# Performance work log

Hardware: AMD Instinct MI355X
Metric: run time of the kernel (lower is better)

The kernel has to match this reference:

```python
import jax, jax.numpy as jnp
import numpy as np

R, H, K, C = 8, 8, 4096, 128  # residual stages, subvectors, codebook size, subvector dim
B, S = 2, 2048


def setup_inputs() -> dict:
    key = jax.random.key(0)
    k1, k2 = jax.random.split(key)
    x = jax.random.normal(k1, (B, S, H * C), dtype=jnp.float32)
    codebook = jax.random.normal(k2, (R, H, K, C), dtype=jnp.float32) * 0.1
    return {"x": x, "codebook": codebook}


def _encode(x, codebook):
    b, s, f = x.shape
    # x.view(b,s,8,2,64).transpose(3,4).flatten(2)  -> interleave the two 64-dim halves per head
    xp = x.reshape(b, s, 8, 2, 64).transpose(0, 1, 2, 4, 3).reshape(b, s, f)
    prescale = jnp.linalg.norm(xp, axis=-1, keepdims=True)  # (b,s,1)
    xn = xp / prescale
    # (b s) h c  -> permute to (h, N, c)
    t0 = xn.reshape(b * s, H, C).transpose(1, 0, 2)  # (H, N, C)

    def step(t, cb_r):
        # cb_r: (H, K, C). Squared-euclidean argmin == torch.cdist argmin (sqrt is monotone,
        # and the ||t||^2 term is constant over k so it is dropped).
        d = jnp.sum(cb_r * cb_r, axis=-1)[:, None, :] - 2.0 * jnp.einsum('hnc,hkc->hnk', t, cb_r)
        idx = jnp.argmin(d, axis=-1)  # (H, N)
        q = jnp.take_along_axis(cb_r, idx[..., None], axis=1)  # (H, N, C)
        return t - q, idx.astype(jnp.int32)

    _, codes = jax.lax.scan(step, t0, codebook)  # codes: (R, H, N)
    return codes, prescale


def _decode(codes, prescale, codebook):
    # gather codebook entries: (R, H, N, C)
    g = jnp.take_along_axis(codebook, codes[..., None], axis=2)
    n = codes.shape[2]
    # permute(0,2,1,3).flatten(-2).sum(0): (R,N,H*C) summed over residual stages
    rec = g.transpose(0, 2, 1, 3).reshape(R, n, H * C).sum(0)  # (N, H*C)
    b = prescale.shape[0]
    return rec.reshape(b, -1, H * C) * prescale


def reference(x, codebook):
    codes, prescale = _encode(x, codebook)
    return _decode(codes, prescale, codebook)
```

## Files before the change

### kernel.cpp

```cpp
#include <hip/hip_runtime.h>

#define R_STAGES 8
#define H_HEADS  8
#define K_CODES  4096
#define C_DIM    128
#define N_TOK    4096
#define FEAT     1024
#define HKC      (H_HEADS * K_CODES * C_DIM)

#define MARGIN   1e-2f
#define PCAP     16

typedef _Float16 half8  __attribute__((ext_vector_type(8)));
typedef _Float16 half4v __attribute__((ext_vector_type(4)));
typedef float    f32x4  __attribute__((ext_vector_type(4)));

#define MFMA16(A, B, C) __builtin_amdgcn_mfma_f32_16x16x32_f16((A), (B), (C), 0, 0, 0)


__global__ void kc_prep(const float* __restrict__ x, float* __restrict__ t,
                        float* __restrict__ ps) {
    int n = blockIdx.x;
    const float* xr = x + (size_t)n * FEAT;

    double ss = 0.0;
    for (int i = threadIdx.x; i < FEAT; i += 256) {
        float v = xr[i];
        ss += (double)v * (double)v;
    }
    for (int off = 32; off > 0; off >>= 1) ss += __shfl_down(ss, off);

    __shared__ double sred[4];
    __shared__ float s_p;
    int wid = threadIdx.x >> 6, lane = threadIdx.x & 63;
    if (lane == 0) sred[wid] = ss;
    __syncthreads();
    if (threadIdx.x == 0) {
        double tot = sred[0] + sred[1] + sred[2] + sred[3];
        float p = (float)sqrt(tot);
        ps[n] = p;
        s_p = p;
    }
    __syncthreads();
    float p = s_p;

    for (int i = threadIdx.x; i < FEAT; i += 256) {
        int c = i & 127;
        float v = xr[(i & ~127) + ((c & 1) << 6) + (c >> 1)];
        size_t o = ((size_t)(i >> 7) * N_TOK + n) * C_DIM + c;
        t[o] = v / p;
    }
}

__global__ void kc_cbn(const float* __restrict__ cb, float* __restrict__ cn) {
    int w = (blockIdx.x << 2) + (threadIdx.x >> 6);
    int lane = threadIdx.x & 63;
    const float* row = cb + (size_t)w * C_DIM;
    float a = row[lane], b = row[lane + 64];
    double s = (double)a * a + (double)b * b;
    for (int off = 32; off > 0; off >>= 1) s += __shfl_down(s, off);
    if (lane == 0) cn[w] = (float)s;
}

__global__ void kc_cvt(const float* __restrict__ s, _Float16* __restrict__ d, int n4) {
    int i = blockIdx.x * 256 + threadIdx.x;
    if (i < n4) {
        f32x4 v = ((const f32x4*)s)[i];
        half4v o;
        o[0] = (_Float16)v[0]; o[1] = (_Float16)v[1];
        o[2] = (_Float16)v[2]; o[3] = (_Float16)v[3];
        ((half4v*)d)[i] = o;
    }
}

__global__ __launch_bounds__(256, 2)
void kc_stage(const float* __restrict__ cb32, const _Float16* __restrict__ cb16,
              const float* __restrict__ cn, float* __restrict__ t) {
    __shared__ float  rbs[256][4];
    __shared__ float  mtok[64];
    __shared__ int    pcnt[64];
    __shared__ int    plist[64][PCAP];
    __shared__ int    winner[64];
    __shared__ double redD[256];
    __shared__ int    redI[256];

    const int tid  = threadIdx.x;
    const int w    = tid >> 6;
    const int lane = tid & 63;
    const int col  = lane & 15;
    const int rblk = lane >> 4;
    const int h    = blockIdx.x & 7;
    const int n0   = (blockIdx.x >> 3) << 6;

    const _Float16* cbh16 = cb16 + (size_t)h * K_CODES * C_DIM;
    const float*    cbh32 = cb32 + (size_t)h * K_CODES * C_DIM;
    const float*    cnh   = cn   + (size_t)h * K_CODES;
    float* th = t + ((size_t)h * N_TOK + n0) * C_DIM;

    if (tid < 64) pcnt[tid] = 0;

    half8 tf[4][4];
#pragma unroll
    for (int g = 0; g < 4; ++g) {
        const float* trow = th + (size_t)(g * 16 + col) * C_DIM;
#pragma unroll
        for (int j = 0; j < 4; ++j) {
            const float* p = trow + j * 32 + rblk * 8;
            f32x4 lo = *(const f32x4*)p;
            f32x4 hi = *(const f32x4*)(p + 4);
            half8 v;
            v[0] = (_Float16)lo[0]; v[1] = (_Float16)lo[1];
            v[2] = (_Float16)lo[2]; v[3] = (_Float16)lo[3];
            v[4] = (_Float16)hi[0]; v[5] = (_Float16)hi[1];
            v[6] = (_Float16)hi[2]; v[7] = (_Float16)hi[3];
            tf[g][j] = v;
        }
    }

    const int kbase = w << 10;
    const _Float16* cbA = cbh16 + (size_t)(kbase + col) * C_DIM + rblk * 8;
    const float*    cnA = cnh + kbase + (rblk << 2);

    auto loadA = [&](int it, half8* A, f32x4& cv) {
        const _Float16* p = cbA + (size_t)it * (16 * C_DIM);
#pragma unroll
        for (int j = 0; j < 4; ++j) A[j] = *(const half8*)(p + j * 32);
        cv = *(const f32x4*)(cnA + it * 16);
    };

    float rb0 = 3.4e38f, rb1 = 3.4e38f, rb2 = 3.4e38f, rb3 = 3.4e38f;

    auto screen = [&](const half8* A, const f32x4& cv) {
        f32x4 a0 = {0.f,0.f,0.f,0.f}, a1 = {0.f,0.f,0.f,0.f};
        f32x4 a2 = {0.f,0.f,0.f,0.f}, a3 = {0.f,0.f,0.f,0.f};
#pragma unroll
        for (int j = 0; j < 4; ++j) {
            a0 = MFMA16(A[j], tf[0][j], a0);
            a1 = MFMA16(A[j], tf[1][j], a1);
            a2 = MFMA16(A[j], tf[2][j], a2);
            a3 = MFMA16(A[j], tf[3][j], a3);
        }
        {
            float d0 = cv[0] - 2.f*a0[0], d1 = cv[1] - 2.f*a0[1];
            float d2 = cv[2] - 2.f*a0[2], d3 = cv[3] - 2.f*a0[3];
            rb0 = fminf(rb0, fminf(fminf(d0, d1), fminf(d2, d3)));
        }
        {
            float d0 = cv[0] - 2.f*a1[0], d1 = cv[1] - 2.f*a1[1];
            float d2 = cv[2] - 2.f*a1[2], d3 = cv[3] - 2.f*a1[3];
            rb1 = fminf(rb1, fminf(fminf(d0, d1), fminf(d2, d3)));
        }
        {
            float d0 = cv[0] - 2.f*a2[0], d1 = cv[1] - 2.f*a2[1];
            float d2 = cv[2] - 2.f*a2[2], d3 = cv[3] - 2.f*a2[3];
            rb2 = fminf(rb2, fminf(fminf(d0, d1), fminf(d2, d3)));
        }
        {
            float d0 = cv[0] - 2.f*a3[0], d1 = cv[1] - 2.f*a3[1];
            float d2 = cv[2] - 2.f*a3[2], d3 = cv[3] - 2.f*a3[3];
            rb3 = fminf(rb3, fminf(fminf(d0, d1), fminf(d2, d3)));
        }
    };

    {
        half8 X[4], Y[4]; f32x4 cx, cy;
        loadA(0, X, cx);
#pragma unroll 1
        for (int it = 0; it < 64; it += 2) {
            loadA(it + 1, Y, cy);
            screen(X, cx);
            if (it + 2 < 64) loadA(it + 2, X, cx);
            screen(Y, cy);
        }
    }

    rbs[tid][0] = rb0; rbs[tid][1] = rb1; rbs[tid][2] = rb2; rbs[tid][3] = rb3;
    __syncthreads();
    if (tid < 64) {
        int g = tid >> 4, c2 = tid & 15;
        float m = 3.4e38f;
#pragma unroll
        for (int ww = 0; ww < 4; ++ww)
#pragma unroll
            for (int rr = 0; rr < 4; ++rr)
                m = fminf(m, rbs[ww * 64 + rr * 16 + c2][g]);
        mtok[tid] = m;
    }
    __syncthreads();

    const float thr0 = mtok[col]      + MARGIN;
    const float thr1 = mtok[16 + col] + MARGIN;
    const float thr2 = mtok[32 + col] + MARGIN;
    const float thr3 = mtok[48 + col] + MARGIN;

    auto collect = [&](const half8* A, const f32x4& cv, int it) {
        f32x4 a0 = {0.f,0.f,0.f,0.f}, a1 = {0.f,0.f,0.f,0.f};
        f32x4 a2 = {0.f,0.f,0.f,0.f}, a3 = {0.f,0.f,0.f,0.f};
#pragma unroll
        for (int j = 0; j < 4; ++j) {
            a0 = MFMA16(A[j], tf[0][j], a0);
            a1 = MFMA16(A[j], tf[1][j], a1);
            a2 = MFMA16(A[j], tf[2][j], a2);
            a3 = MFMA16(A[j], tf[3][j], a3);
        }
        const int kb2 = kbase + it * 16 + (rblk << 2);
#pragma unroll
        for (int rr = 0; rr < 4; ++rr) {
            float d0 = cv[rr] - 2.f * a0[rr];
            float d1 = cv[rr] - 2.f * a1[rr];
            float d2 = cv[rr] - 2.f * a2[rr];
            float d3 = cv[rr] - 2.f * a3[rr];
            if (d0 < thr0) { int idx = atomicAdd(&pcnt[col],      1); if (idx < PCAP) plist[col][idx]      = kb2 + rr; }
            if (d1 < thr1) { int idx = atomicAdd(&pcnt[16 + col], 1); if (idx < PCAP) plist[16 + col][idx] = kb2 + rr; }
            if (d2 < thr2) { int idx = atomicAdd(&pcnt[32 + col], 1); if (idx < PCAP) plist[32 + col][idx] = kb2 + rr; }
            if (d3 < thr3) { int idx = atomicAdd(&pcnt[48 + col], 1); if (idx < PCAP) plist[48 + col][idx] = kb2 + rr; }
        }
    };

    {
        half8 X[4], Y[4]; f32x4 cx, cy;
        loadA(0, X, cx);
#pragma unroll 1
        for (int it = 0; it < 64; it += 2) {
            loadA(it + 1, Y, cy);
            collect(X, cx, it);
            if (it + 2 < 64) loadA(it + 2, X, cx);
            collect(Y, cy, it + 1);
        }
    }
    __syncthreads();

    {
        const int tok = tid >> 2, q = tid & 3;
        int m = pcnt[tok]; if (m > PCAP) m = PCAP;
        const float* trw = th + (size_t)tok * C_DIM;
        double bd = 1e300; int bi = 0x7fffffff;
        for (int e = q; e < m; e += 4) {
            const int k = plist[tok][e];
            const float* crow = cbh32 + (size_t)k * C_DIM;
            double dot = 0.0, cx2 = 0.0;
            for (int c = 0; c < C_DIM; ++c) {
                double cvv = (double)crow[c];
                double tvv = (double)trw[c];
                cx2 = fma(cvv, cvv, cx2);
                dot = fma(tvv, cvv, dot);
            }
            double d = cx2 - 2.0 * dot;
            if (d < bd || (d == bd && k < bi)) { bd = d; bi = k; }
        }
        redD[tid] = bd; redI[tid] = bi;
    }
    __syncthreads();
    if ((tid & 3) == 0) {
        const int tok = tid >> 2;
        double bd = redD[tid]; int bi = redI[tid];
#pragma unroll
        for (int q = 1; q < 4; ++q) {
            double d = redD[tid + q]; int i2 = redI[tid + q];
            if (d < bd || (d == bd && i2 < bi)) { bd = d; bi = i2; }
        }
        winner[tok] = bi;
    }
    __syncthreads();

    for (int ot = 0; ot < 64; ++ot) {
        if (pcnt[ot] <= PCAP) continue;
        const float* trw = th + (size_t)ot * C_DIM;
        double bd = 1e300; int bi = 0x7fffffff;
        for (int k = tid; k < K_CODES; k += 256) {
            const float* crow = cbh32 + (size_t)k * C_DIM;
            double dot = 0.0, cx2 = 0.0;
            for (int c = 0; c < C_DIM; ++c) {
                double cvv = (double)crow[c];
                double tvv = (double)trw[c];
                cx2 = fma(cvv, cvv, cx2);
                dot = fma(tvv, cvv, dot);
            }
            double d = cx2 - 2.0 * dot;
            if (d < bd || (d == bd && k < bi)) { bd = d; bi = k; }
        }
        for (int off = 32; off > 0; off >>= 1) {
            double od = __shfl_down(bd, off);
            int    oi = __shfl_down(bi, off);
            if (od < bd || (od == bd && oi < bi)) { bd = od; bi = oi; }
        }
        if (lane == 0) { redD[w] = bd; redI[w] = bi; }
        __syncthreads();
        if (tid == 0) {
            double b2 = redD[0]; int i2 = redI[0];
            for (int q = 1; q < 4; ++q) {
                if (redD[q] < b2 || (redD[q] == b2 && redI[q] < i2)) {
                    b2 = redD[q]; i2 = redI[q];
                }
            }
            winner[ot] = i2;
        }
        __syncthreads();
    }

    for (int i = tid; i < 64 * C_DIM; i += 256) {
        const int tok = i >> 7, c = i & 127;
        const float qv = cbh32[(size_t)winner[tok] * C_DIM + c];
        th[(size_t)tok * C_DIM + c] -= qv;
    }
}

__global__ void kc_out(const float* __restrict__ x, const float* __restrict__ t,
                       const float* __restrict__ ps, float* __restrict__ out) {
    int n = blockIdx.x;
    float p = ps[n];
    const float* xr = x + (size_t)n * FEAT;
    for (int i = threadIdx.x; i < FEAT; i += 256) {
        int c = i & 127;
        float v = xr[(i & ~127) + ((c & 1) << 6) + (c >> 1)];
        float t0 = v / p;
        float tf = t[((size_t)(i >> 7) * N_TOK + n) * C_DIM + c];
        out[(size_t)n * FEAT + i] = (t0 - tf) * p;
    }
}

extern "C" void kernel_launch(void* const* d_in, const int* in_sizes, int n_in,
                              void* d_out, int out_size, void* d_ws, size_t ws_size,
                              hipStream_t stream) {
    const float* x  = (const float*)d_in[0];
    const float* cb = (const float*)d_in[1];
    float* out = (float*)d_out;

    float*    t    = (float*)d_ws;
    float*    ps   = (float*)((char*)d_ws + 16777216);
    float*    cn   = (float*)((char*)d_ws + 16793600);
    _Float16* cb16 = (_Float16*)((char*)d_ws + 17842176);

    const bool full = (ws_size >= 51500000ull);

    kc_prep<<<N_TOK, 256, 0, stream>>>(x, t, ps);
    kc_cbn<<<(R_STAGES * H_HEADS * K_CODES) / 4, 256, 0, stream>>>(cb, cn);
    if (full) {
        const int n4 = R_STAGES * HKC / 4;
        kc_cvt<<<(n4 + 255) / 256, 256, 0, stream>>>(cb, cb16, n4);
    }

    for (int r = 0; r < R_STAGES; ++r) {
        const _Float16* cb16s;
        if (full) {
            cb16s = cb16 + (size_t)r * HKC;
        } else {
            const int n4 = HKC / 4;
            kc_cvt<<<(n4 + 255) / 256, 256, 0, stream>>>(cb + (size_t)r * HKC, cb16, n4);
            cb16s = cb16;
        }
        kc_stage<<<H_HEADS * (N_TOK / 64), 256, 0, stream>>>(
            cb + (size_t)r * HKC, cb16s,
            cn + (size_t)r * H_HEADS * K_CODES, t);
    }
    kc_out<<<N_TOK, 256, 0, stream>>>(x, t, ps, out);
}
```

Baseline: 1.223 ms.

## Replace second MFMA pass with per-tile min cache and fuse all stages into one kernel

The screening pass now stores a per-16-code-tile minimum distance for each token in shared memory. Candidate tiles are then picked from that cache instead of recomputing all distances in a second MFMA collect pass, and only those tiles are rescored in double precision. All residual stages run inside one persistent kernel per token-block, removing per-stage launches, and codebook fp16 conversion is fused with norm computation. This adds a large shared-memory buffer, which may reduce occupancy. It also falls back to full brute-force rescoring whenever the candidate list overflows.

```diff
diff --git a/kernel.cpp b/kernel.cpp
--- a/kernel.cpp
+++ b/kernel.cpp
@@ -8,8 +8,9 @@
 #define FEAT     1024
 #define HKC      (H_HEADS * K_CODES * C_DIM)
 
-#define MARGIN   1e-2f
-#define PCAP     16
+#define MARGIN   1.2e-2f
+#define WCAP     512
+#define TMS      260
 
 typedef _Float16 half8  __attribute__((ext_vector_type(8)));
 typedef _Float16 half4v __attribute__((ext_vector_type(4)));
@@ -52,52 +53,40 @@
     }
 }
 
-__global__ void kc_cbn(const float* __restrict__ cb, float* __restrict__ cn) {
+__global__ void kc_cvtn(const float* __restrict__ cb, _Float16* __restrict__ cb16,
+                        float* __restrict__ cn) {
     int w = (blockIdx.x << 2) + (threadIdx.x >> 6);
     int lane = threadIdx.x & 63;
     const float* row = cb + (size_t)w * C_DIM;
     float a = row[lane], b = row[lane + 64];
+    _Float16* dr = cb16 + (size_t)w * C_DIM;
+    dr[lane]      = (_Float16)a;
+    dr[lane + 64] = (_Float16)b;
     double s = (double)a * a + (double)b * b;
     for (int off = 32; off > 0; off >>= 1) s += __shfl_down(s, off);
     if (lane == 0) cn[w] = (float)s;
 }
 
-__global__ void kc_cvt(const float* __restrict__ s, _Float16* __restrict__ d, int n4) {
-    int i = blockIdx.x * 256 + threadIdx.x;
-    if (i < n4) {
-        f32x4 v = ((const f32x4*)s)[i];
-        half4v o;
-        o[0] = (_Float16)v[0]; o[1] = (_Float16)v[1];
-        o[2] = (_Float16)v[2]; o[3] = (_Float16)v[3];
-        ((half4v*)d)[i] = o;
-    }
-}
-
-__global__ __launch_bounds__(256, 2)
-void kc_stage(const float* __restrict__ cb32, const _Float16* __restrict__ cb16,
-              const float* __restrict__ cn, float* __restrict__ t) {
-    __shared__ float  rbs[256][4];
-    __shared__ float  mtok[64];
-    __shared__ int    pcnt[64];
-    __shared__ int    plist[64][PCAP];
-    __shared__ int    winner[64];
-    __shared__ double redD[256];
-    __shared__ int    redI[256];
+__device__ __forceinline__ void stage_body(
+    const float* __restrict__ cbh32, const _Float16* __restrict__ cbh16,
+    const float* __restrict__ cnh, float* __restrict__ th) {
+
+    __shared__ _Float16 tmin[64 * TMS];
+    __shared__ float    rbs[256][4];
+    __shared__ float    mtok[64];
+    __shared__ int      wl[WCAP];
+    __shared__ double   eD[WCAP];
+    __shared__ int      eI[WCAP];
+    __shared__ int      winner[64];
+    __shared__ int      wlCnt;
 
     const int tid  = threadIdx.x;
     const int w    = tid >> 6;
     const int lane = tid & 63;
     const int col  = lane & 15;
     const int rblk = lane >> 4;
-    const int h    = blockIdx.x & 7;
-    const int n0   = (blockIdx.x >> 3) << 6;
-
-    const _Float16* cbh16 = cb16 + (size_t)h * K_CODES * C_DIM;
-    const float*    cbh32 = cb32 + (size_t)h * K_CODES * C_DIM;
-    const float*    cnh   = cn   + (size_t)h * K_CODES;
-    float* th = t + ((size_t)h * N_TOK + n0) * C_DIM;
-
-    if (tid < 64) pcnt[tid] = 0;
+
+    if (tid == 0) wlCnt = 0;
 
     half8 tf[4][4];
 #pragma unroll
@@ -128,9 +117,9 @@
         cv = *(const f32x4*)(cnA + it * 16);
     };
 
-    float rb0 = 3.4e38f, rb1 = 3.4e38f, rb2 = 3.4e38f, rb3 = 3.4e38f;
-
-    auto screen = [&](const half8* A, const f32x4& cv) {
+    float rbg0 = 3.4e38f, rbg1 = 3.4e38f, rbg2 = 3.4e38f, rbg3 = 3.4e38f;
+
+    auto screen = [&](const half8* A, const f32x4& cv, int wtile) {
         f32x4 a0 = {0.f,0.f,0.f,0.f}, a1 = {0.f,0.f,0.f,0.f};
         f32x4 a2 = {0.f,0.f,0.f,0.f}, a3 = {0.f,0.f,0.f,0.f};
 #pragma unroll
@@ -140,169 +129,188 @@
             a2 = MFMA16(A[j], tf[2][j], a2);
             a3 = MFMA16(A[j], tf[3][j], a3);
         }
-        {
-            float d0 = cv[0] - 2.f*a0[0], d1 = cv[1] - 2.f*a0[1];
-            float d2 = cv[2] - 2.f*a0[2], d3 = cv[3] - 2.f*a0[3];
-            rb0 = fminf(rb0, fminf(fminf(d0, d1), fminf(d2, d3)));
-        }
-        {
-            float d0 = cv[0] - 2.f*a1[0], d1 = cv[1] - 2.f*a1[1];
-            float d2 = cv[2] - 2.f*a1[2], d3 = cv[3] - 2.f*a1[3];
-            rb1 = fminf(rb1, fminf(fminf(d0, d1), fminf(d2, d3)));
-        }
-        {
-            float d0 = cv[0] - 2.f*a2[0], d1 = cv[1] - 2.f*a2[1];
-            float d2 = cv[2] - 2.f*a2[2], d3 = cv[3] - 2.f*a2[3];
-            rb2 = fminf(rb2, fminf(fminf(d0, d1), fminf(d2, d3)));
-        }
-        {
-            float d0 = cv[0] - 2.f*a3[0], d1 = cv[1] - 2.f*a3[1];
-            float d2 = cv[2] - 2.f*a3[2], d3 = cv[3] - 2.f*a3[3];
-            rb3 = fminf(rb3, fminf(fminf(d0, d1), fminf(d2, d3)));
+        float m0 = fminf(fminf(cv[0] - 2.f*a0[0], cv[1] - 2.f*a0[1]),
+                         fminf(cv[2] - 2.f*a0[2], cv[3] - 2.f*a0[3]));
+        float m1 = fminf(fminf(cv[0] - 2.f*a1[0], cv[1] - 2.f*a1[1]),
+                         fminf(cv[2] - 2.f*a1[2], cv[3] - 2.f*a1[3]));
+        float m2 = fminf(fminf(cv[0] - 2.f*a2[0], cv[1] - 2.f*a2[1]),
+                         fminf(cv[2] - 2.f*a2[2], cv[3] - 2.f*a2[3]));
+        float m3 = fminf(fminf(cv[0] - 2.f*a3[0], cv[1] - 2.f*a3[1]),
+                         fminf(cv[2] - 2.f*a3[2], cv[3] - 2.f*a3[3]));
+        m0 = fminf(m0, __shfl_xor(m0, 16)); m0 = fminf(m0, __shfl_xor(m0, 32));
+        m1 = fminf(m1, __shfl_xor(m1, 16)); m1 = fminf(m1, __shfl_xor(m1, 32));
+        m2 = fminf(m2, __shfl_xor(m2, 16)); m2 = fminf(m2, __shfl_xor(m2, 32));
+        m3 = fminf(m3, __shfl_xor(m3, 16)); m3 = fminf(m3, __shfl_xor(m3, 32));
+        rbg0 = fminf(rbg0, m0); rbg1 = fminf(rbg1, m1);
+        rbg2 = fminf(rbg2, m2); rbg3 = fminf(rbg3, m3);
+        if (rblk == 0) {
+            tmin[(col)      * TMS + wtile] = (_Float16)m0;
+            tmin[(16 + col) * TMS + wtile] = (_Float16)m1;
+            tmin[(32 + col) * TMS + wtile] = (_Float16)m2;
+            tmin[(48 + col) * TMS + wtile] = (_Float16)m3;
         }
     };
 
     {
-        half8 X[4], Y[4]; f32x4 cx, cy;
-        loadA(0, X, cx);
+        half8 A0[4], A1[4], A2[4], A3[4];
+        f32x4 v0, v1, v2, v3;
+        loadA(0, A0, v0); loadA(1, A1, v1); loadA(2, A2, v2); loadA(3, A3, v3);
+        const int wbase = w << 6;
 #pragma unroll 1
-        for (int it = 0; it < 64; it += 2) {
-            loadA(it + 1, Y, cy);
-            screen(X, cx);
-            if (it + 2 < 64) loadA(it + 2, X, cx);
-            screen(Y, cy);
-        }
-    }
-
-    rbs[tid][0] = rb0; rbs[tid][1] = rb1; rbs[tid][2] = rb2; rbs[tid][3] = rb3;
-    __syncthreads();
+        for (int j = 0; j < 16; ++j) {
+            const int b4 = j << 2;
+            screen(A0, v0, wbase + b4);
+            if (j < 15) loadA(b4 + 4, A0, v0);
+            screen(A1, v1, wbase + b4 + 1);
+            if (j < 15) loadA(b4 + 5, A1, v1);
+            screen(A2, v2, wbase + b4 + 2);
+            if (j < 15) loadA(b4 + 6, A2, v2);
+            screen(A3, v3, wbase + b4 + 3);
+            if (j < 15) loadA(b4 + 7, A3, v3);
+        }
+    }
+    rbs[tid][0] = rbg0; rbs[tid][1] = rbg1; rbs[tid][2] = rbg2; rbs[tid][3] = rbg3;
+    __syncthreads();
+
     if (tid < 64) {
-        int g = tid >> 4, c2 = tid & 15;
+        const int g = tid >> 4, c2 = tid & 15;
         float m = 3.4e38f;
 #pragma unroll
-        for (int ww = 0; ww < 4; ++ww)
-#pragma unroll
-            for (int rr = 0; rr < 4; ++rr)
-                m = fminf(m, rbs[ww * 64 + rr * 16 + c2][g]);
+        for (int ww = 0; ww < 4; ++ww) m = fminf(m, rbs[ww * 64 + c2][g]);
         mtok[tid] = m;
-    }
-    __syncthreads();
-
-    const float thr0 = mtok[col]      + MARGIN;
-    const float thr1 = mtok[16 + col] + MARGIN;
-    const float thr2 = mtok[32 + col] + MARGIN;
-    const float thr3 = mtok[48 + col] + MARGIN;
-
-    auto collect = [&](const half8* A, const f32x4& cv, int it) {
-        f32x4 a0 = {0.f,0.f,0.f,0.f}, a1 = {0.f,0.f,0.f,0.f};
-        f32x4 a2 = {0.f,0.f,0.f,0.f}, a3 = {0.f,0.f,0.f,0.f};
-#pragma unroll
-        for (int j = 0; j < 4; ++j) {
-            a0 = MFMA16(A[j], tf[0][j], a0);
-            a1 = MFMA16(A[j], tf[1][j], a1);
-            a2 = MFMA16(A[j], tf[2][j], a2);
-            a3 = MFMA16(A[j], tf[3][j], a3);
-        }
-        const int kb2 = kbase + it * 16 + (rblk << 2);
-#pragma unroll
-        for (int rr = 0; rr < 4; ++rr) {
-            float d0 = cv[rr] - 2.f * a0[rr];
-            float d1 = cv[rr] - 2.f * a1[rr];
-            float d2 = cv[rr] - 2.f * a2[rr];
-            float d3 = cv[rr] - 2.f * a3[rr];
-            if (d0 < thr0) { int idx = atomicAdd(&pcnt[col],      1); if (idx < PCAP) plist[col][idx]      = kb2 + rr; }
-            if (d1 < thr1) { int idx = atomicAdd(&pcnt[16 + col], 1); if (idx < PCAP) plist[16 + col][idx] = kb2 + rr; }
-            if (d2 < thr2) { int idx = atomicAdd(&pcnt[32 + col], 1); if (idx < PCAP) plist[32 + col][idx] = kb2 + rr; }
-            if (d3 < thr3) { int idx = atomicAdd(&pcnt[48 + col], 1); if (idx < PCAP) plist[48 + col][idx] = kb2 + rr; }
-        }
-    };
-
-    {
-        half8 X[4], Y[4]; f32x4 cx, cy;
-        loadA(0, X, cx);
-#pragma unroll 1
-        for (int it = 0; it < 64; it += 2) {
-            loadA(it + 1, Y, cy);
-            collect(X, cx, it);
-            if (it + 2 < 64) loadA(it + 2, X, cx);
-            collect(Y, cy, it + 1);
-        }
     }
     __syncthreads();
 
     {
         const int tok = tid >> 2, q = tid & 3;
-        int m = pcnt[tok]; if (m > PCAP) m = PCAP;
-        const float* trw = th + (size_t)tok * C_DIM;
-        double bd = 1e300; int bi = 0x7fffffff;
-        for (int e = q; e < m; e += 4) {
-            const int k = plist[tok][e];
-            const float* crow = cbh32 + (size_t)k * C_DIM;
-            double dot = 0.0, cx2 = 0.0;
-            for (int c = 0; c < C_DIM; ++c) {
-                double cvv = (double)crow[c];
-                double tvv = (double)trw[c];
-                cx2 = fma(cvv, cvv, cx2);
-                dot = fma(tvv, cvv, dot);
-            }
-            double d = cx2 - 2.0 * dot;
-            if (d < bd || (d == bd && k < bi)) { bd = d; bi = k; }
-        }
-        redD[tid] = bd; redI[tid] = bi;
-    }
-    __syncthreads();
-    if ((tid & 3) == 0) {
-        const int tok = tid >> 2;
-        double bd = redD[tid]; int bi = redI[tid];
-#pragma unroll
-        for (int q = 1; q < 4; ++q) {
-            double d = redD[tid + q]; int i2 = redI[tid + q];
-            if (d < bd || (d == bd && i2 < bi)) { bd = d; bi = i2; }
-        }
-        winner[tok] = bi;
-    }
-    __syncthreads();
-
-    for (int ot = 0; ot < 64; ++ot) {
-        if (pcnt[ot] <= PCAP) continue;
-        const float* trw = th + (size_t)ot * C_DIM;
-        double bd = 1e300; int bi = 0x7fffffff;
-        for (int k = tid; k < K_CODES; k += 256) {
-            const float* crow = cbh32 + (size_t)k * C_DIM;
-            double dot = 0.0, cx2 = 0.0;
-            for (int c = 0; c < C_DIM; ++c) {
-                double cvv = (double)crow[c];
-                double tvv = (double)trw[c];
-                cx2 = fma(cvv, cvv, cx2);
-                dot = fma(tvv, cvv, dot);
-            }
-            double d = cx2 - 2.0 * dot;
-            if (d < bd || (d == bd && k < bi)) { bd = d; bi = k; }
-        }
-        for (int off = 32; off > 0; off >>= 1) {
-            double od = __shfl_down(bd, off);
-            int    oi = __shfl_down(bi, off);
-            if (od < bd || (od == bd && oi < bi)) { bd = od; bi = oi; }
-        }
-        if (lane == 0) { redD[w] = bd; redI[w] = bi; }
+        const float thr = mtok[tok] + MARGIN;
+        const half4v* rowp = (const half4v*)(tmin + tok * TMS + (q << 6));
+#pragma unroll 4
+        for (int j4 = 0; j4 < 16; ++j4) {
+            half4v v = rowp[j4];
+#pragma unroll
+            for (int e = 0; e < 4; ++e) {
+                if ((float)v[e] < thr) {
+                    int idx = atomicAdd(&wlCnt, 1);
+                    if (idx < WCAP) wl[idx] = (tok << 8) | ((q << 6) + (j4 << 2) + e);
+                }
+            }
+        }
+    }
+    __syncthreads();
+
+    int E = wlCnt;
+    if (E <= WCAP) {
+        for (int e0 = 0; e0 < E; e0 += 16) {
+            const int e = e0 + (tid >> 4);
+            double bd = 1e300; int bi = 0x7fffffff;
+            if (e < E) {
+                const int meta = wl[e];
+                const int tok = meta >> 8;
+                const int k = ((meta & 255) << 4) + (tid & 15);
+                const float* crow = cbh32 + (size_t)k * C_DIM;
+                const float* trw  = th + (size_t)tok * C_DIM;
+                double cx0=0,cx1=0,cx2=0,cx3=0,d0=0,d1=0,d2=0,d3=0;
+#pragma unroll 4
+                for (int c = 0; c < C_DIM; c += 4) {
+                    double cv0 = crow[c],   tv0 = trw[c];
+                    double cv1 = crow[c+1], tv1 = trw[c+1];
+                    double cv2 = crow[c+2], tv2 = trw[c+2];
+                    double cv3 = crow[c+3], tv3 = trw[c+3];
+                    cx0 = fma(cv0,cv0,cx0); d0 = fma(tv0,cv0,d0);
+                    cx1 = fma(cv1,cv1,cx1); d1 = fma(tv1,cv1,d1);
+                    cx2 = fma(cv2,cv2,cx2); d2 = fma(tv2,cv2,d2);
+                    cx3 = fma(cv3,cv3,cx3); d3 = fma(tv3,cv3,d3);
+                }
+                bd = ((cx0+cx1)+(cx2+cx3)) - 2.0*((d0+d1)+(d2+d3));
+                bi = k;
+            }
+#pragma unroll
+            for (int off = 1; off < 16; off <<= 1) {
+                double od = __shfl_xor(bd, off);
+                int    oi = __shfl_xor(bi, off);
+                if (od < bd || (od == bd && oi < bi)) { bd = od; bi = oi; }
+            }
+            if ((tid & 15) == 0 && e < E) { eD[e >> 0] = bd; eI[e] = bi; }
+        }
         __syncthreads();
-        if (tid == 0) {
-            double b2 = redD[0]; int i2 = redI[0];
-            for (int q = 1; q < 4; ++q) {
-                if (redD[q] < b2 || (redD[q] == b2 && redI[q] < i2)) {
-                    b2 = redD[q]; i2 = redI[q];
-                }
-            }
-            winner[ot] = i2;
+        if (tid < 64) {
+            double bd = 1e300; int bi = 0x7fffffff;
+            for (int e = 0; e < E; ++e) {
+                if ((wl[e] >> 8) == tid) {
+                    double d = eD[e]; int i2 = eI[e];
+                    if (d < bd || (d == bd && i2 < bi)) { bd = d; bi = i2; }
+                }
+            }
+            winner[tid] = bi;
         }
         __syncthreads();
+    } else {
+        for (int ot = 0; ot < 64; ++ot) {
+            const float* trw = th + (size_t)ot * C_DIM;
+            double bd = 1e300; int bi = 0x7fffffff;
+            for (int k = tid; k < K_CODES; k += 256) {
+                const float* crow = cbh32 + (size_t)k * C_DIM;
+                double cx0=0,cx1=0,cx2=0,cx3=0,d0=0,d1=0,d2=0,d3=0;
+                for (int c = 0; c < C_DIM; c += 4) {
+                    double cv0 = crow[c],   tv0 = trw[c];
+                    double cv1 = crow[c+1], tv1 = trw[c+1];
+                    double cv2 = crow[c+2], tv2 = trw[c+2];
+                    double cv3 = crow[c+3], tv3 = trw[c+3];
+                    cx0 = fma(cv0,cv0,cx0); d0 = fma(tv0,cv0,d0);
+                    cx1 = fma(cv1,cv1,cx1); d1 = fma(tv1,cv1,d1);
+                    cx2 = fma(cv2,cv2,cx2); d2 = fma(tv2,cv2,d2);
+                    cx3 = fma(cv3,cv3,cx3); d3 = fma(tv3,cv3,d3);
+                }
+                double d = ((cx0+cx1)+(cx2+cx3)) - 2.0*((d0+d1)+(d2+d3));
+                if (d < bd || (d == bd && k < bi)) { bd = d; bi = k; }
+            }
+            for (int off = 1; off <= 32; off <<= 1) {
+                double od = __shfl_xor(bd, off);
+                int    oi = __shfl_xor(bi, off);
+                if (od < bd || (od == bd && oi < bi)) { bd = od; bi = oi; }
+            }
+            if (lane == 0) { eD[w] = bd; eI[w] = bi; }
+            __syncthreads();
+            if (tid == 0) {
+                double b2 = eD[0]; int i2 = eI[0];
+                for (int q = 1; q < 4; ++q) {
+                    if (eD[q] < b2 || (eD[q] == b2 && eI[q] < i2)) { b2 = eD[q]; i2 = eI[q]; }
+                }
+                winner[ot] = i2;
+            }
+            __syncthreads();
+        }
     }
 
     for (int i = tid; i < 64 * C_DIM; i += 256) {
         const int tok = i >> 7, c = i & 127;
-        const float qv = cbh32[(size_t)winner[tok] * C_DIM + c];
-        th[(size_t)tok * C_DIM + c] -= qv;
-    }
+        th[(size_t)tok * C_DIM + c] -= cbh32[(size_t)winner[tok] * C_DIM + c];
+    }
+    __syncthreads();
+}
+
+__global__ __launch_bounds__(256, 2)
+void kc_all(const float* __restrict__ cb32, const _Float16* __restrict__ cb16,
+            const float* __restrict__ cn, float* __restrict__ t) {
+    const int h  = blockIdx.x & 7;
+    const int n0 = (blockIdx.x >> 3) << 6;
+    float* th = t + ((size_t)h * N_TOK + n0) * C_DIM;
+#pragma unroll 1
+    for (int r = 0; r < R_STAGES; ++r) {
+        const size_t off = (size_t)(r * H_HEADS + h) * K_CODES;
+        stage_body(cb32 + off * C_DIM, cb16 + off * C_DIM, cn + off, th);
+    }
+}
+
+__global__ __launch_bounds__(256, 2)
+void kc_stage_one(const float* __restrict__ cb32, const _Float16* __restrict__ cb16,
+                  const float* __restrict__ cn, float* __restrict__ t) {
+    const int h  = blockIdx.x & 7;
+    const int n0 = (blockIdx.x >> 3) << 6;
+    float* th = t + ((size_t)h * N_TOK + n0) * C_DIM;
+    const size_t off = (size_t)h * K_CODES;
+    stage_body(cb32 + off * C_DIM, cb16 + off * C_DIM, cn + off, th);
 }
 
 __global__ void kc_out(const float* __restrict__ x, const float* __restrict__ t,
@@ -331,27 +339,21 @@
     float*    cn   = (float*)((char*)d_ws + 16793600);
     _Float16* cb16 = (_Float16*)((char*)d_ws + 17842176);
 
-    const bool full = (ws_size >= 51500000ull);
+    const bool full = (ws_size >= 84951040ull);
 
     kc_prep<<<N_TOK, 256, 0, stream>>>(x, t, ps);
-    kc_cbn<<<(R_STAGES * H_HEADS * K_CODES) / 4, 256, 0, stream>>>(cb, cn);
+
     if (full) {
-        const int n4 = R_STAGES * HKC / 4;
-        kc_cvt<<<(n4 + 255) / 256, 256, 0, stream>>>(cb, cb16, n4);
-    }
-
-    for (int r = 0; r < R_STAGES; ++r) {
-        const _Float16* cb16s;
-        if (full) {
-            cb16s = cb16 + (size_t)r * HKC;
-        } else {
-            const int n4 = HKC / 4;
-            kc_cvt<<<(n4 + 255) / 256, 256, 0, stream>>>(cb + (size_t)r * HKC, cb16, n4);
-            cb16s = cb16;
-        }
-        kc_stage<<<H_HEADS * (N_TOK / 64), 256, 0, stream>>>(
-            cb + (size_t)r * HKC, cb16s,
-            cn + (size_t)r * H_HEADS * K_CODES, t);
-    }
+        kc_cvtn<<<(R_STAGES * H_HEADS * K_CODES) / 4, 256, 0, stream>>>(cb, cb16, cn);
+        kc_all<<<H_HEADS * (N_TOK / 64), 256, 0, stream>>>(cb, cb16, cn, t);
+    } else {
+        for (int r = 0; r < R_STAGES; ++r) {
+            kc_cvtn<<<(H_HEADS * K_CODES) / 4, 256, 0, stream>>>(
+                cb + (size_t)r * HKC, cb16, cn + (size_t)r * H_HEADS * K_CODES);
+            kc_stage_one<<<H_HEADS * (N_TOK / 64), 256, 0, stream>>>(
+                cb + (size_t)r * HKC, cb16, cn + (size_t)r * H_HEADS * K_CODES, t);
+        }
+    }
+
     kc_out<<<N_TOK, 256, 0, stream>>>(x, t, ps, out);
 }
```

Result: faster. 1.063 ms (-13.1%).
